# Kernel optimization log

Hardware: AMD Instinct MI355X
Metric: run time of the kernel (lower is better)

The kernel has to match this reference:

```python
import jax, jax.numpy as jnp
import numpy as np

EMBED_DIM = 2048
NUM_HEADS = 16
NUM_HEADS_KV = 16
HEAD_DIM = EMBED_DIM // NUM_HEADS  # 128
ROT_DIM = HEAD_DIM // 2            # rotary_emb_dim = 64 (partial rotary)
ROPE_BASE = 10000.0
SEQLEN = 2048


def _rope_cos_sin(seqlen):
    # inv_freq over rotary dim (fp32 positions, as pos_idx_in_fp32=True)
    inv_freq = 1.0 / (ROPE_BASE ** (jnp.arange(0, ROT_DIM, 2, dtype=jnp.float32) / ROT_DIM))
    t = jnp.arange(seqlen, dtype=jnp.float32)
    freqs = jnp.outer(t, inv_freq)                 # (S, ROT_DIM//2)
    return jnp.cos(freqs), jnp.sin(freqs)


def _apply_rotary(x, cos, sin):
    # x: (B, S, H, D); non-interleaved (GPT-NeoX) rotary on first ROT_DIM dims
    rd = cos.shape[-1] * 2
    x_rot, x_pass = x[..., :rd], x[..., rd:]
    x1, x2 = x_rot[..., : rd // 2], x_rot[..., rd // 2 :]
    c = cos[None, :, None, :]
    s = sin[None, :, None, :]
    o1 = x1 * c - x2 * s
    o2 = x1 * s + x2 * c
    return jnp.concatenate([o1, o2, x_pass], axis=-1)


def setup_inputs() -> dict:
    key = jax.random.key(0)
    ks = jax.random.split(key, 5)
    scale_in = 1.0 / np.sqrt(EMBED_DIM)
    return {
        "x_q": jax.random.normal(ks[0], (SEQLEN, EMBED_DIM), dtype=jnp.float32),
        "Wqkv_w": jax.random.normal(ks[1], (HEAD_DIM * (NUM_HEADS + 2 * NUM_HEADS_KV), EMBED_DIM), dtype=jnp.float32) * scale_in,
        "Wqkv_b": jax.random.normal(ks[2], (HEAD_DIM * (NUM_HEADS + 2 * NUM_HEADS_KV),), dtype=jnp.float32) * 0.01,
        "Wo_w": jax.random.normal(ks[3], (EMBED_DIM, EMBED_DIM), dtype=jnp.float32) * scale_in,
        "Wo_b": jax.random.normal(ks[4], (EMBED_DIM,), dtype=jnp.float32) * 0.01,
    }


def reference(x_q, Wqkv_w, Wqkv_b, Wo_w, Wo_b):
    S = x_q.shape[0]
    H, Hkv, D = NUM_HEADS, NUM_HEADS_KV, HEAD_DIM
    # fused QKV projection
    qkv = x_q @ Wqkv_w.T + Wqkv_b                     # (S, (H+2Hkv)*D)
    q = qkv[:, : H * D].reshape(1, S, H, D)
    kv = qkv[:, H * D :].reshape(1, S, 2, Hkv, D)
    # rotary (q_position_ids = k_position_ids = arange(S))
    cos, sin = _rope_cos_sin(S)
    q = _apply_rotary(q, cos, sin)
    k = _apply_rotary(kv[:, :, 0], cos, sin)          # (1, S, Hkv, D)
    v = kv[:, :, 1]
    # causal attention, softmax scale 1/sqrt(D)
    scores = jnp.einsum("bshd,bthd->bhst", q, k) / jnp.sqrt(jnp.float32(D))
    causal = jnp.arange(S)[:, None] >= jnp.arange(S)[None, :]  # (S, S)
    scores = jnp.where(causal[None, None], scores, jnp.float32(-1e30))
    attn = jax.nn.softmax(scores, axis=-1)
    out = jnp.einsum("bhst,bthd->bshd", attn, v)      # (1, S, H, D)
    out = out.reshape(1, S, H * D)
    out = out @ Wo_w.T + Wo_b
    return out[0]                                     # (S, E)
```

## Files before the change

### kernel.cpp

```cpp
#include <hip/hip_runtime.h>
#include <stdint.h>

#define QKV_N 6144
#define ATT_SCALE 0.08838834764831845f

typedef __attribute__((ext_vector_type(8))) short short8;
typedef __attribute__((ext_vector_type(4))) float f32x4;

__device__ __forceinline__ uint16_t f2b(float x){
  uint32_t u = __float_as_uint(x);
  uint32_t r = (u + 0x7fffu + ((u >> 16) & 1u)) >> 16;
  return (uint16_t)r;
}
__device__ __forceinline__ float b2f(uint16_t h){
  return __uint_as_float(((uint32_t)h) << 16);
}
__device__ __forceinline__ void g2l16(const void* g, void* l){
  __builtin_amdgcn_global_load_lds((const __attribute__((address_space(1))) void*)g,
                                   (__attribute__((address_space(3))) void*)l, 16, 0, 0);
}

__device__ __forceinline__ void cvt8(const float* __restrict__ in, uint16_t* __restrict__ out, int i){
  const float4* p = (const float4*)in;
  float4 a = p[2*i], b = p[2*i+1];
  union { short8 v; uint16_t u[8]; } o;
  o.u[0]=f2b(a.x); o.u[1]=f2b(a.y); o.u[2]=f2b(a.z); o.u[3]=f2b(a.w);
  o.u[4]=f2b(b.x); o.u[5]=f2b(b.y); o.u[6]=f2b(b.z); o.u[7]=f2b(b.w);
  ((short8*)out)[i] = o.v;
}

__global__ __launch_bounds__(256) void k_prep(const float* __restrict__ x,
                                              const float* __restrict__ wqkv,
                                              const float* __restrict__ wo,
                                              uint16_t* __restrict__ xb,
                                              uint16_t* __restrict__ wqkvb,
                                              uint16_t* __restrict__ wob,
                                              float* __restrict__ ct,
                                              float* __restrict__ st){
  const int b = blockIdx.x, tid = threadIdx.x;
  if (b < 2048) {
    cvt8(x, xb, b*256 + tid);
  } else if (b < 8192) {
    cvt8(wqkv, wqkvb, (b - 2048)*256 + tid);
  } else if (b < 10240) {
    cvt8(wo, wob, (b - 8192)*256 + tid);
  } else {
    int i = (b - 10240)*256 + tid;
    int s = i >> 5, d = i & 31;
    float inv = __expf(-(float)d * (9.210340371976184f / 32.0f));
    float f = (float)s * inv;
    ct[i] = cosf(f);
    st[i] = sinf(f);
  }
}

__global__ __launch_bounds__(512, 1) void k_gemmA(const uint16_t* __restrict__ A,
                                                  const uint16_t* __restrict__ B,
                                                  const float* __restrict__ bias,
                                                  uint16_t* __restrict__ C){
  __shared__ uint16_t As[3*4096];
  __shared__ uint16_t Bs[3*6144];
  const int K = 2048, N = 6144;

  const int wg = blockIdx.x;
  const int xcd = wg & 7, bi = wg >> 3;
  const int m0 = (xcd*2 + (bi & 1)) * 128;
  const int n0 = (bi >> 1) * 192;

  const int tid = threadIdx.x;
  const int wid = tid >> 6, l = tid & 63;
  const int wm = wid >> 2, wn = wid & 3;
  const int g = l >> 4, c = l & 15;

  const int rpA = tid >> 3, sA = (tid & 7) ^ (rpA & 7);
  const size_t srcA0 = (size_t)(m0 + rpA*2 + (sA >> 2)) * K + (sA & 3) * 8;
  const size_t srcB0 = (size_t)(n0 + rpA*2 + (sA >> 2)) * K + (sA & 3) * 8;
  const int rpB2 = 64 + (tid >> 3), sB2 = (tid & 7) ^ (rpB2 & 7);
  const size_t srcB1 = (size_t)(n0 + rpB2*2 + (sB2 >> 2)) * K + (sB2 & 3) * 8;

  const int pg   = ((c & 1) << 2) | g;
  const int slb  = (pg ^ ((c >> 1) & 7)) << 3;
  const int rpa0 = wm*32 + (c >> 1);
  const int rpb0 = wn*24 + (c >> 1);

  f32x4 acc[4][3] = {};
  const int NT = K >> 5;

  #pragma unroll
  for (int t0 = 0; t0 < 2; ++t0) {
    g2l16(A + srcA0 + t0*32, (void*)(As + t0*4096 + tid*8));
    g2l16(B + srcB0 + t0*32, (void*)(Bs + t0*6144 + tid*8));
    if (tid < 256)
      g2l16(B + srcB1 + t0*32, (void*)(Bs + t0*6144 + 4096 + tid*8));
  }
  if (wid < 4) { asm volatile("s_waitcnt vmcnt(3)" ::: "memory"); }
  else         { asm volatile("s_waitcnt vmcnt(2)" ::: "memory"); }
  __builtin_amdgcn_s_barrier();

  #pragma unroll 3
  for (int t = 0; t < NT; ++t) {
    const uint16_t* __restrict__ Ab = As + (t % 3)*4096;
    const uint16_t* __restrict__ Bb = Bs + (t % 3)*6144;
    const int t2 = t + 2;

    short8 av[4], bv[3];
    #pragma unroll
    for (int mi = 0; mi < 4; ++mi)
      av[mi] = *(const short8*)&Ab[(rpa0 + mi*8)*64 + slb];
    #pragma unroll
    for (int ni = 0; ni < 3; ++ni)
      bv[ni] = *(const short8*)&Bb[(rpb0 + ni*8)*64 + slb];
    if (t2 < NT) {
      const int b2 = (t2 % 3);
      g2l16(A + srcA0 + t2*32, (void*)(As + b2*4096 + tid*8));
      g2l16(B + srcB0 + t2*32, (void*)(Bs + b2*6144 + tid*8));
      if (tid < 256)
        g2l16(B + srcB1 + t2*32, (void*)(Bs + b2*6144 + 4096 + tid*8));
    }
    __builtin_amdgcn_s_barrier();
    __builtin_amdgcn_s_setprio(1);
    #pragma unroll
    for (int mi = 0; mi < 4; ++mi)
      #pragma unroll
      for (int ni = 0; ni < 3; ++ni)
        acc[mi][ni] = __builtin_amdgcn_mfma_f32_16x16x32_bf16(av[mi], bv[ni], acc[mi][ni], 0, 0, 0);
    __builtin_amdgcn_s_setprio(0);
    if (wid < 4) { asm volatile("s_waitcnt vmcnt(3)" ::: "memory"); }
    else         { asm volatile("s_waitcnt vmcnt(2)" ::: "memory"); }
    __builtin_amdgcn_s_barrier();
  }

  #pragma unroll
  for (int ni = 0; ni < 3; ++ni) {
    const int col = n0 + wn*48 + ni*16 + c;
    const float bvl = bias[col];
    #pragma unroll
    for (int mi = 0; mi < 4; ++mi) {
      const int row0 = m0 + wm*64 + mi*16 + g*4;
      #pragma unroll
      for (int j = 0; j < 4; ++j)
        C[(size_t)(row0 + j)*N + col] = f2b(acc[mi][ni][j] + bvl);
    }
  }
}

__global__ __launch_bounds__(512, 1) void k_gemm128(const uint16_t* __restrict__ A,
                                                    const uint16_t* __restrict__ B,
                                                    const float* __restrict__ bias,
                                                    float* __restrict__ C,
                                                    int M, int N, int K){
  __shared__ uint16_t As[4*4096];
  __shared__ uint16_t Bs[4*4096];

  const int wg = blockIdx.x;
  const int xcd = wg & 7, bi = wg >> 3;
  const int m0 = (xcd*2 + (bi & 1)) * 128;
  const int n0 = (bi >> 1) * 128;

  const int tid = threadIdx.x;
  const int wid = tid >> 6, l = tid & 63;
  const int wm = wid >> 2, wn = wid & 3;
  const int g = l >> 4, c = l & 15;

  const int rp_s = tid >> 3, q_s = tid & 7, s_s = q_s ^ (rp_s & 7);
  const int srcA = (m0 + rp_s*2 + (s_s >> 2)) * K + (s_s & 3) * 8;
  const int srcB = (n0 + rp_s*2 + (s_s >> 2)) * K + (s_s & 3) * 8;

  const int pg  = ((c & 1) << 2) | g;
  const int slb = (pg ^ ((c >> 1) & 7)) << 3;
  const int ra0 = wm*32 + (c >> 1);
  const int rb0 = wn*16 + (c >> 1);

  f32x4 acc[4][2] = {};
  const int NT = K >> 5;

  #pragma unroll
  for (int t0 = 0; t0 < 3; ++t0) {
    g2l16(A + srcA + t0*32, (void*)(As + t0*4096 + tid*8));
    g2l16(B + srcB + t0*32, (void*)(Bs + t0*4096 + tid*8));
  }
  asm volatile("s_waitcnt vmcnt(4)" ::: "memory");
  __builtin_amdgcn_s_barrier();

  #pragma unroll 4
  for (int t = 0; t < NT; ++t) {
    const uint16_t* __restrict__ Ab = As + (t & 3)*4096;
    const uint16_t* __restrict__ Bb = Bs + (t & 3)*4096;
    const int t3 = t + 3;
    const int b3 = (t3 & 3)*4096;

    short8 av[4], bv[2];
    #pragma unroll
    for (int mi = 0; mi < 4; ++mi)
      av[mi] = *(const short8*)&Ab[(ra0 + mi*8)*64 + slb];
    #pragma unroll
    for (int ni = 0; ni < 2; ++ni)
      bv[ni] = *(const short8*)&Bb[(rb0 + ni*8)*64 + slb];
    if (t3 < NT) {
      g2l16(A + srcA + t3*32, (void*)(As + b3 + tid*8));
      g2l16(B + srcB + t3*32, (void*)(Bs + b3 + tid*8));
    }
    __builtin_amdgcn_s_barrier();
    __builtin_amdgcn_s_setprio(1);
    #pragma unroll
    for (int mi = 0; mi < 4; ++mi)
      #pragma unroll
      for (int ni = 0; ni < 2; ++ni)
        acc[mi][ni] = __builtin_amdgcn_mfma_f32_16x16x32_bf16(av[mi], bv[ni], acc[mi][ni], 0, 0, 0);
    __builtin_amdgcn_s_setprio(0);
    asm volatile("s_waitcnt vmcnt(4)" ::: "memory");
    __builtin_amdgcn_s_barrier();
  }

  #pragma unroll
  for (int ni = 0; ni < 2; ++ni) {
    const int col = n0 + wn*32 + ni*16 + c;
    const float bvl = bias[col];
    #pragma unroll
    for (int mi = 0; mi < 4; ++mi) {
      const int row0 = m0 + wm*64 + mi*16 + g*4;
      #pragma unroll
      for (int j = 0; j < 4; ++j)
        C[(size_t)(row0 + j)*N + col] = acc[mi][ni][j] + bvl;
    }
  }
}

__global__ __launch_bounds__(256) void k_rope_vt(const uint16_t* __restrict__ qkv,
                                                 const float* __restrict__ ct,
                                                 const float* __restrict__ st,
                                                 uint16_t* __restrict__ qo,
                                                 uint16_t* __restrict__ ko,
                                                 uint16_t* __restrict__ vt){
  const int blk = blockIdx.x, tid = threadIdx.x;
  if (blk < 4096) {
    int idx = blk * 256 + tid;
    int db = idx & 15;
    int s  = (idx >> 4) & 2047;
    int h  = (idx >> 15) & 15;
    int which = idx >> 19;
    const uint16_t* src = qkv + (size_t)s * QKV_N + which * 2048 + h * 128;
    uint16_t* dst = (which ? ko : qo) + (((size_t)(h*2048 + s)) << 7) + db*8;
    const float scale = which ? 1.0f : ATT_SCALE;
    int d0 = db * 8;
    union { short8 v; uint16_t u[8]; } o;
    if (d0 >= 64) {
      short8 xv = *(const short8*)(src + d0);
      #pragma unroll
      for (int e = 0; e < 8; ++e) o.u[e] = f2b(b2f((uint16_t)xv[e]) * scale);
    } else {
      int dd = d0 & 31;
      short8 a = *(const short8*)(src + dd);
      short8 b = *(const short8*)(src + dd + 32);
      float4 c0 = *(const float4*)(ct + s*32 + dd);
      float4 c1 = *(const float4*)(ct + s*32 + dd + 4);
      float4 s0 = *(const float4*)(st + s*32 + dd);
      float4 s1 = *(const float4*)(st + s*32 + dd + 4);
      float cc[8] = {c0.x,c0.y,c0.z,c0.w,c1.x,c1.y,c1.z,c1.w};
      float ss[8] = {s0.x,s0.y,s0.z,s0.w,s1.x,s1.y,s1.z,s1.w};
      #pragma unroll
      for (int e = 0; e < 8; ++e) {
        float x1 = b2f((uint16_t)a[e]), x2 = b2f((uint16_t)b[e]);
        float v = (d0 < 32) ? (x1*cc[e] - x2*ss[e]) : (x1*ss[e] + x2*cc[e]);
        o.u[e] = f2b(v * scale);
      }
    }
    *(short8*)dst = o.v;
  } else {
    __shared__ uint16_t tl[64][80];
    const int b = blk - 4096;
    const int st_ = b & 31, dt = (b >> 5) & 1, h = b >> 6;
    const int s_l = tid >> 2, cch = (tid & 3) * 16;
    const uint16_t* src = qkv + (size_t)(st_*64 + s_l) * QKV_N + 4096 + h*128 + dt*64 + cch;
    short8 a = *(const short8*)src;
    short8 b2 = *(const short8*)(src + 8);
    #pragma unroll
    for (int e = 0; e < 8; ++e) {
      tl[cch + e][s_l]     = (uint16_t)a[e];
      tl[cch + 8 + e][s_l] = (uint16_t)b2[e];
    }
    __syncthreads();
    const int d_l = tid >> 2;
    uint16_t* dst = vt + ((size_t)h << 18) + (size_t)(dt*64 + d_l) * 2048 + st_*64 + cch;
    *(short8*)dst       = *(const short8*)&tl[d_l][cch];
    *(short8*)(dst + 8) = *(const short8*)&tl[d_l][cch + 8];
  }
}

__global__ __launch_bounds__(512, 1) void k_attn(const uint16_t* __restrict__ Q,
                                                 const uint16_t* __restrict__ Kb,
                                                 const uint16_t* __restrict__ Vtg,
                                                 uint16_t* __restrict__ Out){
  __shared__ uint16_t Ks[2][2][64*128];
  __shared__ uint16_t Vs[2][2][128*64];
  __shared__ uint16_t Ps[8][16*88];

  const int bid = blockIdx.x;
  const int lin = (bid & 7) * 32 + (bid >> 3);
  const int h = lin >> 4;
  const int pair = lin & 15;

  const int tid = threadIdx.x, w = tid >> 6, l = tid & 63;
  const int gid = w >> 2, wq = w & 3;
  const int tg = tid & 255;
  const int g = l >> 4, c = l & 15;
  const int swz = (c & 7) << 4;

  const uint16_t* __restrict__ Qh = Q   + ((size_t)h << 18);
  const uint16_t* __restrict__ Kh = Kb  + ((size_t)h << 18);
  const uint16_t* __restrict__ Vh = Vtg + ((size_t)h << 18);
  float* scratch = (float*)&Ks[0][0][0];

  int koff[4], voff[4];
  #pragma unroll
  for (int j = 0; j < 4; ++j) {
    int kr = j*16 + (tg >> 4);
    koff[j] = kr*128 + (((tg & 15) ^ (kr & 7)) << 3);
    int vd = j*32 + (tg >> 3);
    voff[j] = vd*2048 + (((tg & 7) ^ (vd & 7)) << 3);
  }

  uint16_t* KsG = &Ks[gid][0][0];
  uint16_t* VsG = &Vs[gid][0][0];

  #pragma unroll 1
  for (int half = 0; half < 2; ++half) {
    const int qt = half ? (31 - pair) : pair;
    const int nt = qt + 1;
    const int nsteps = (nt + 1) >> 1;
    const int qrow = qt*64 + wq*16 + c;

    short8 qf[4];
    #pragma unroll
    for (int t = 0; t < 4; ++t)
      qf[t] = *(const short8*)&Qh[(size_t)qrow*128 + t*32 + g*8];

    f32x4 acc[8] = {};
    float mrow[4], lsum[4];
    #pragma unroll
    for (int j = 0; j < 4; ++j) { mrow[j] = -3e38f; lsum[j] = 0.0f; }

    if (gid < nt) {
      #pragma unroll
      for (int j = 0; j < 4; ++j) {
        g2l16(Kh + (size_t)gid*8192 + koff[j], (void*)(KsG + j*2048 + tg*8));
        g2l16(Vh + gid*64 + voff[j],           (void*)(VsG + j*2048 + tg*8));
      }
    }
    asm volatile("s_waitcnt vmcnt(0)" ::: "memory");
    __syncthreads();

    #pragma unroll 1
    for (int step = 0; step < nsteps; ++step) {
      const int kt = 2*step + gid;
      const int cur = step & 1;
      if (kt + 2 < nt) {
        const int k1 = kt + 2;
        #pragma unroll
        for (int j = 0; j < 4; ++j) {
          g2l16(Kh + (size_t)k1*8192 + koff[j], (void*)(KsG + (cur^1)*8192 + j*2048 + tg*8));
          g2l16(Vh + k1*64 + voff[j],           (void*)(VsG + (cur^1)*8192 + j*2048 + tg*8));
        }
      }

      if (kt < nt) {
        const int k0 = kt * 64;
        const uint16_t* Kcur = KsG + cur*8192;
        const uint16_t* Vcur = VsG + cur*8192;

        f32x4 sc4[4] = {};
        __builtin_amdgcn_s_setprio(1);
        #pragma unroll
        for (int ct2 = 0; ct2 < 4; ++ct2) {
          const char* krp = (const char*)Kcur + (ct2*16 + c)*256;
          #pragma unroll
          for (int t = 0; t < 4; ++t) {
            short8 kb = *(const short8*)(krp + ((t*64 + g*16) ^ swz));
            sc4[ct2] = __builtin_amdgcn_mfma_f32_16x16x32_bf16(qf[t], kb, sc4[ct2], 0, 0, 0);
          }
        }
        __builtin_amdgcn_s_setprio(0);

        const bool lastt = (kt == nt - 1);
        float va[4][4];
        float m4[4];
        int fastok = 1;
        #pragma unroll
        for (int j = 0; j < 4; ++j) {
          const int qg = qt*64 + wq*16 + g*4 + j;
          float v0 = sc4[0][j], v1 = sc4[1][j], v2 = sc4[2][j], v3 = sc4[3][j];
          if (lastt) {
            if (k0 +      c > qg) v0 = -3e38f;
            if (k0 + 16 + c > qg) v1 = -3e38f;
            if (k0 + 32 + c > qg) v2 = -3e38f;
            if (k0 + 48 + c > qg) v3 = -3e38f;
          }
          va[j][0] = v0; va[j][1] = v1; va[j][2] = v2; va[j][3] = v3;
          float m = fmaxf(fmaxf(fmaxf(v0, v1), v2), v3);
          m4[j] = m;
          fastok &= (m <= mrow[j] + 8.0f) ? 1 : 0;
        }
        if (__all(fastok)) {
          #pragma unroll
          for (int j = 0; j < 4; ++j) {
            const float mj = mrow[j];
            const float p0 = __expf(va[j][0] - mj), p1 = __expf(va[j][1] - mj),
                        p2 = __expf(va[j][2] - mj), p3 = __expf(va[j][3] - mj);
            lsum[j] += (p0 + p1) + (p2 + p3);
            uint16_t* pw = &Ps[w][(g*4 + j)*88];
            pw[c] = f2b(p0); pw[16+c] = f2b(p1); pw[32+c] = f2b(p2); pw[48+c] = f2b(p3);
          }
        } else {
          #pragma unroll
          for (int j = 0; j < 4; ++j) {
            float t0 = m4[j];
            #pragma unroll
            for (int d2 = 1; d2 < 16; d2 <<= 1) t0 = fmaxf(t0, __shfl_xor(t0, d2, 64));
            const float mn = fmaxf(mrow[j], t0);
            const float scl = __expf(mrow[j] - mn);
            const float p0 = __expf(va[j][0] - mn), p1 = __expf(va[j][1] - mn),
                        p2 = __expf(va[j][2] - mn), p3 = __expf(va[j][3] - mn);
            lsum[j] = lsum[j]*scl + (p0 + p1) + (p2 + p3);
            mrow[j] = mn;
            #pragma unroll
            for (int n = 0; n < 8; ++n) acc[n][j] *= scl;
            uint16_t* pw = &Ps[w][(g*4 + j)*88];
            pw[c] = f2b(p0); pw[16+c] = f2b(p1); pw[32+c] = f2b(p2); pw[48+c] = f2b(p3);
          }
        }

        __builtin_amdgcn_s_setprio(1);
        #pragma unroll
        for (int kk = 0; kk < 2; ++kk) {
          short8 pf = *(const short8*)&Ps[w][c*88 + kk*32 + g*8];
          #pragma unroll
          for (int n = 0; n < 8; ++n) {
            const char* vrp = (const char*)Vcur + (n*16 + c)*128;
            short8 vf = *(const short8*)(vrp + ((kk*64 + g*16) ^ swz));
            acc[n] = __builtin_amdgcn_mfma_f32_16x16x32_bf16(pf, vf, acc[n], 0, 0, 0);
          }
        }
        __builtin_amdgcn_s_setprio(0);
      }

      asm volatile("s_waitcnt vmcnt(0)" ::: "memory");
      __syncthreads();
    }

    float lrow[4];
    #pragma unroll
    for (int j = 0; j < 4; ++j) {
      float rs = lsum[j];
      #pragma unroll
      for (int d2 = 1; d2 < 16; d2 <<= 1) rs += __shfl_xor(rs, d2, 64);
      lrow[j] = rs;
    }

    float* Up = scratch + wq * 2112;
    if (gid == 1) {
      #pragma unroll
      for (int j = 0; j < 4; ++j) {
        const int row = g*4 + j;
        #pragma unroll
        for (int n = 0; n < 8; ++n)
          Up[row*128 + n*16 + c] = acc[n][j];
        if (c == 0) { Up[2048 + row] = mrow[j]; Up[2064 + row] = lrow[j]; }
      }
    }
    __syncthreads();
    if (gid == 0) {
      #pragma unroll
      for (int j = 0; j < 4; ++j) {
        const int row = g*4 + j;
        const int qg = qt*64 + wq*16 + row;
        const float mB = Up[2048 + row], lB = Up[2064 + row];
        const float mn = fmaxf(mrow[j], mB);
        const float e1 = __expf(mrow[j] - mn);
        const float e2 = __expf(mB - mn);
        const float inv = 1.0f / (lrow[j]*e1 + lB*e2);
        #pragma unroll
        for (int n = 0; n < 8; ++n) {
          const float u = acc[n][j]*e1 + Up[row*128 + n*16 + c]*e2;
          Out[(size_t)qg*2048 + h*128 + n*16 + c] = f2b(u * inv);
        }
      }
    }
    __syncthreads();
  }
}

extern "C" void kernel_launch(void* const* d_in, const int* in_sizes, int n_in,
                              void* d_out, int out_size, void* d_ws, size_t ws_size,
                              hipStream_t stream){
  const float* x    = (const float*)d_in[0];
  const float* Wqkv = (const float*)d_in[1];
  const float* bqkv = (const float*)d_in[2];
  const float* Wo   = (const float*)d_in[3];
  const float* bo   = (const float*)d_in[4];

  char* ws = (char*)d_ws;
  uint16_t* q_bf    = (uint16_t*)(ws);
  uint16_t* k_bf    = (uint16_t*)(ws + 8388608);
  uint16_t* vt_bf   = (uint16_t*)(ws + 16777216);
  uint16_t* attn_bf = (uint16_t*)(ws + 25165824);
  uint16_t* x_bf    = attn_bf;
  uint16_t* wqkv_bf = (uint16_t*)(ws + 33554432);
  uint16_t* wo_bf   = (uint16_t*)(ws + 58720256);
  uint16_t* qkv_bf  = (uint16_t*)(ws + 67108864);
  float*    cos_t   = (float*)(ws + 92274688);
  float*    sin_t   = (float*)(ws + 92536832);

  k_prep<<<dim3(10496), dim3(256), 0, stream>>>(x, Wqkv, Wo, x_bf, wqkv_bf, wo_bf,
                                                cos_t, sin_t);
  k_gemmA<<<dim3(512), dim3(512), 0, stream>>>(x_bf, wqkv_bf, bqkv, qkv_bf);
  k_rope_vt<<<dim3(5120), dim3(256), 0, stream>>>(qkv_bf, cos_t, sin_t, q_bf, k_bf, vt_bf);
  k_attn<<<dim3(256), dim3(512), 0, stream>>>(q_bf, k_bf, vt_bf, attn_bf);
  k_gemm128<<<dim3(256), dim3(512), 0, stream>>>(attn_bf, wo_bf, bo, (float*)d_out,
                                                 2048, 2048, 2048);
}
```

Measured before the change: 165.2 us.

## Restructure QKV GEMM to double-buffered K=64 tiles with one barrier per step

Changes the QKV projection GEMM from a three-stage pipeline with K=32 tiles to a two-stage double buffer with K=64 tiles. Each iteration now has a single barrier instead of two, and a new XOR swizzle on the LDS layout. Each tile is loaded as whole 64-element rows, and every loaded A/B fragment now feeds two MFMAs. The aim is to halve loop iterations and barrier overhead and to raise MFMA work per sync. In exchange, prefetch depth drops to one tile and each step waits with vmcnt(0), which may expose more global-load latency.

```diff
diff --git a/kernel.cpp b/kernel.cpp
--- a/kernel.cpp
+++ b/kernel.cpp
@@ -58,8 +58,7 @@
                                                   const uint16_t* __restrict__ B,
                                                   const float* __restrict__ bias,
                                                   uint16_t* __restrict__ C){
-  __shared__ uint16_t As[3*4096];
-  __shared__ uint16_t Bs[3*6144];
+  __shared__ uint16_t Ls[2*20480];
   const int K = 2048, N = 6144;
 
   const int wg = blockIdx.x;
@@ -72,61 +71,72 @@
   const int wm = wid >> 2, wn = wid & 3;
   const int g = l >> 4, c = l & 15;
 
-  const int rpA = tid >> 3, sA = (tid & 7) ^ (rpA & 7);
-  const size_t srcA0 = (size_t)(m0 + rpA*2 + (sA >> 2)) * K + (sA & 3) * 8;
-  const size_t srcB0 = (size_t)(n0 + rpA*2 + (sA >> 2)) * K + (sA & 3) * 8;
-  const int rpB2 = 64 + (tid >> 3), sB2 = (tid & 7) ^ (rpB2 & 7);
-  const size_t srcB1 = (size_t)(n0 + rpB2*2 + (sB2 >> 2)) * K + (sB2 & 3) * 8;
-
-  const int pg   = ((c & 1) << 2) | g;
-  const int slb  = (pg ^ ((c >> 1) & 7)) << 3;
-  const int rpa0 = wm*32 + (c >> 1);
-  const int rpb0 = wn*24 + (c >> 1);
+  size_t srcA[2]; int dstA[2];
+  #pragma unroll
+  for (int j = 0; j < 2; ++j) {
+    int f = tid + 512*j, r = f >> 3, q = f & 7;
+    srcA[j] = (size_t)(m0 + r) * K + ((q ^ (r & 7)) << 3);
+    dstA[j] = f * 8;
+  }
+  size_t srcB[3]; int dstB[3];
+  #pragma unroll
+  for (int j = 0; j < 3; ++j) {
+    int f = tid + 512*j, r = f >> 3, q = f & 7;
+    srcB[j] = (size_t)(n0 + r) * K + ((q ^ (r & 7)) << 3);
+    dstB[j] = 8192 + f * 8;
+  }
+
+  const int sl0 = ((g)     ^ (c & 7)) << 3;
+  const int sl1 = ((4 | g) ^ (c & 7)) << 3;
+  const int arow = (wm*64 + c) * 64;
+  const int brow = 8192 + (wn*48 + c) * 64;
 
   f32x4 acc[4][3] = {};
-  const int NT = K >> 5;
-
-  #pragma unroll
-  for (int t0 = 0; t0 < 2; ++t0) {
-    g2l16(A + srcA0 + t0*32, (void*)(As + t0*4096 + tid*8));
-    g2l16(B + srcB0 + t0*32, (void*)(Bs + t0*6144 + tid*8));
-    if (tid < 256)
-      g2l16(B + srcB1 + t0*32, (void*)(Bs + t0*6144 + 4096 + tid*8));
-  }
-  if (wid < 4) { asm volatile("s_waitcnt vmcnt(3)" ::: "memory"); }
-  else         { asm volatile("s_waitcnt vmcnt(2)" ::: "memory"); }
+  const int NT = K >> 6;
+
+  #pragma unroll
+  for (int j = 0; j < 2; ++j) g2l16(A + srcA[j], (void*)(Ls + dstA[j]));
+  #pragma unroll
+  for (int j = 0; j < 3; ++j) g2l16(B + srcB[j], (void*)(Ls + dstB[j]));
+  asm volatile("s_waitcnt vmcnt(0)" ::: "memory");
   __builtin_amdgcn_s_barrier();
 
-  #pragma unroll 3
+  #pragma unroll 2
   for (int t = 0; t < NT; ++t) {
-    const uint16_t* __restrict__ Ab = As + (t % 3)*4096;
-    const uint16_t* __restrict__ Bb = Bs + (t % 3)*6144;
-    const int t2 = t + 2;
-
-    short8 av[4], bv[3];
+    const uint16_t* __restrict__ Lb = Ls + (t & 1)*20480;
+    uint16_t* __restrict__ Ln = Ls + ((t + 1) & 1)*20480;
+
+    short8 a[4][2], b[3][2];
+    #pragma unroll
+    for (int mi = 0; mi < 4; ++mi) {
+      a[mi][0] = *(const short8*)&Lb[arow + mi*1024 + sl0];
+      a[mi][1] = *(const short8*)&Lb[arow + mi*1024 + sl1];
+    }
+    #pragma unroll
+    for (int ni = 0; ni < 3; ++ni) {
+      b[ni][0] = *(const short8*)&Lb[brow + ni*1024 + sl0];
+      b[ni][1] = *(const short8*)&Lb[brow + ni*1024 + sl1];
+    }
+
+    if (t + 1 < NT) {
+      const size_t ko = (size_t)(t + 1) * 64;
+      #pragma unroll
+      for (int j = 0; j < 2; ++j) g2l16(A + srcA[j] + ko, (void*)(Ln + dstA[j]));
+      #pragma unroll
+      for (int j = 0; j < 3; ++j) g2l16(B + srcB[j] + ko, (void*)(Ln + dstB[j]));
+    }
+
+    __builtin_amdgcn_s_setprio(1);
     #pragma unroll
     for (int mi = 0; mi < 4; ++mi)
-      av[mi] = *(const short8*)&Ab[(rpa0 + mi*8)*64 + slb];
-    #pragma unroll
-    for (int ni = 0; ni < 3; ++ni)
-      bv[ni] = *(const short8*)&Bb[(rpb0 + ni*8)*64 + slb];
-    if (t2 < NT) {
-      const int b2 = (t2 % 3);
-      g2l16(A + srcA0 + t2*32, (void*)(As + b2*4096 + tid*8));
-      g2l16(B + srcB0 + t2*32, (void*)(Bs + b2*6144 + tid*8));
-      if (tid < 256)
-        g2l16(B + srcB1 + t2*32, (void*)(Bs + b2*6144 + 4096 + tid*8));
-    }
-    __builtin_amdgcn_s_barrier();
-    __builtin_amdgcn_s_setprio(1);
-    #pragma unroll
-    for (int mi = 0; mi < 4; ++mi)
       #pragma unroll
       for (int ni = 0; ni < 3; ++ni)
-        acc[mi][ni] = __builtin_amdgcn_mfma_f32_16x16x32_bf16(av[mi], bv[ni], acc[mi][ni], 0, 0, 0);
+        #pragma unroll
+        for (int kk = 0; kk < 2; ++kk)
+          acc[mi][ni] = __builtin_amdgcn_mfma_f32_16x16x32_bf16(a[mi][kk], b[ni][kk], acc[mi][ni], 0, 0, 0);
     __builtin_amdgcn_s_setprio(0);
-    if (wid < 4) { asm volatile("s_waitcnt vmcnt(3)" ::: "memory"); }
-    else         { asm volatile("s_waitcnt vmcnt(2)" ::: "memory"); }
+
+    asm volatile("s_waitcnt vmcnt(0)" ::: "memory");
     __builtin_amdgcn_s_barrier();
   }
 
```

New measurement: 161.6 us (median of 2 runs). 2.2% less time.
